# Kernel tuning notes

Measured on AMD Instinct MI355X. Metric: run time of the kernel, lower is better.

Reference implementation:

```python
import jax, jax.numpy as jnp
import numpy as np

B, S, H = 8, 1024, 16
DV = 1024      # video_input_dim
LAT = 1024     # latent_dim
DQ = LAT // H  # query_dim = 64
DH = 64        # head_dim


def setup_inputs() -> dict:
    key = jax.random.key(0)
    ks = jax.random.split(key, 12)
    sc = lambda fan_in: 1.0 / np.sqrt(fan_in)
    return {
        "input": jax.random.normal(ks[0], (B, S, DV), jnp.float32),
        "latent": jax.random.normal(ks[1], (B, S, LAT), jnp.float32),
        "attention_mask": jax.random.randint(ks[2], (B * H, S, S), 0, 2, jnp.int32),
        "Wq": jax.random.normal(ks[3], (LAT, H * DQ), jnp.float32) * sc(LAT),
        "bq": jnp.zeros((H * DQ,), jnp.float32),
        "Wk": jax.random.normal(ks[4], (DV, H * DQ), jnp.float32) * sc(DV),
        "bk": jnp.zeros((H * DQ,), jnp.float32),
        "Wv": jax.random.normal(ks[5], (DV, H * DH), jnp.float32) * sc(DV),
        "bv": jnp.zeros((H * DH,), jnp.float32),
        "Wo": jax.random.normal(ks[6], (H * DH, LAT), jnp.float32) * sc(H * DH),
        "bo": jnp.zeros((LAT,), jnp.float32),
    }


def reference(input, latent, attention_mask, Wq, bq, Wk, bk, Wv, bv, Wo, bo):
    b, s, _ = input.shape
    # projections -> [b, h, s, d]
    q = (latent @ Wq + bq).reshape(b, s, H, DQ).transpose(0, 2, 1, 3)
    k = (input @ Wk + bk).reshape(b, s, H, DQ).transpose(0, 2, 1, 3)
    v = (input @ Wv + bv).reshape(b, s, H, DH).transpose(0, 2, 1, 3)
    # [b, h, s, s] score matrix (materialized, as in the original bmm)
    scores = jnp.einsum("bhqd,bhkd->bhqk", q, k) / jnp.sqrt(jnp.float32(DQ))
    mask = attention_mask.reshape(b, H, s, s)
    scores = jnp.where(mask == 0, -jnp.inf, scores)
    weights = jax.nn.softmax(scores, axis=-1)
    out = jnp.einsum("bhqk,bhkd->bhqd", weights, v)  # [b, h, s, dh]
    out = out.transpose(0, 2, 1, 3).reshape(b, s, H * DH)
    return out @ Wo + bo
```

## Files before the change

### kernel.cpp

```cpp
#include <hip/hip_runtime.h>
#include <hip/hip_bf16.h>
#include <stdint.h>

typedef __bf16 bf16;
typedef __bf16 bf16x8 __attribute__((ext_vector_type(8)));
typedef float f32x4 __attribute__((ext_vector_type(4)));
typedef unsigned short u16;
typedef unsigned short u16x4 __attribute__((ext_vector_type(4)));


__global__ void convert_f32_bf16(const float* __restrict__ s0, bf16* __restrict__ d0,
                                 const float* __restrict__ s1, bf16* __restrict__ d1) {
    const float* src = blockIdx.y ? s1 : s0;
    bf16* dst = blockIdx.y ? d1 : d0;
    const int nchunk = (8 * 1024 * 1024) / 4;
    for (int c = blockIdx.x * blockDim.x + threadIdx.x; c < nchunk;
         c += gridDim.x * blockDim.x) {
        float4 v = *(const float4*)&src[(size_t)c * 4];
        u16x4 o;
        o[0] = __builtin_bit_cast(u16, (bf16)v.x);
        o[1] = __builtin_bit_cast(u16, (bf16)v.y);
        o[2] = __builtin_bit_cast(u16, (bf16)v.z);
        o[3] = __builtin_bit_cast(u16, (bf16)v.w);
        *(u16x4*)&dst[(size_t)c * 4] = o;
    }
}

__global__ void transpose4(const float* __restrict__ w0, const float* __restrict__ w1,
                           const float* __restrict__ w2, const float* __restrict__ w3,
                           bf16* __restrict__ t0, bf16* __restrict__ t1,
                           bf16* __restrict__ t2, bf16* __restrict__ t3) {
    __shared__ float tile[32][33];
    const float* src; bf16* dst;
    switch (blockIdx.z) {
        case 0:  src = w0; dst = t0; break;
        case 1:  src = w1; dst = t1; break;
        case 2:  src = w2; dst = t2; break;
        default: src = w3; dst = t3; break;
    }
    int tx = threadIdx.x, ty = threadIdx.y;
    int x = blockIdx.x * 32 + tx;
    int y = blockIdx.y * 32 + ty;
    #pragma unroll
    for (int j = 0; j < 32; j += 8)
        tile[ty + j][tx] = src[(size_t)(y + j) * 1024 + x];
    __syncthreads();
    int x2 = blockIdx.y * 32 + tx;
    int y2 = blockIdx.x * 32 + ty;
    #pragma unroll
    for (int j = 0; j < 32; j += 8)
        dst[(size_t)(y2 + j) * 1024 + x2] = (bf16)tile[tx][ty + j];
}

template<int MODE>
__global__ __launch_bounds__(256) void gemm_bt(const bf16* __restrict__ X,
                                               const bf16* __restrict__ Wt,
                                               const float* __restrict__ bias,
                                               void* __restrict__ outv) {
    __shared__ bf16 Al[128 * 40];
    __shared__ bf16 Bl[128 * 40];
    const int tid  = threadIdx.x;
    const int m0   = blockIdx.x * 128;
    const int n0   = blockIdx.y * 128;
    const int lane = tid & 63;
    const int wid  = tid >> 6;
    const int wm   = (wid & 1) * 64;
    const int wn   = (wid >> 1) * 64;
    const int l15  = lane & 15;
    const int quad = lane >> 4;

    f32x4 acc[4][4] = {};

    for (int kt = 0; kt < 1024; kt += 32) {
        __syncthreads();
        for (int c = tid; c < 512; c += 256) {
            int row = c >> 2, col = c & 3;
            *(bf16x8*)&Al[row * 40 + col * 8] =
                *(const bf16x8*)&X[(size_t)(m0 + row) * 1024 + kt + col * 8];
            *(bf16x8*)&Bl[row * 40 + col * 8] =
                *(const bf16x8*)&Wt[(size_t)(n0 + row) * 1024 + kt + col * 8];
        }
        __syncthreads();
        bf16x8 a[4], b[4];
        #pragma unroll
        for (int i = 0; i < 4; i++)
            a[i] = *(const bf16x8*)&Al[(wm + i * 16 + l15) * 40 + quad * 8];
        #pragma unroll
        for (int j = 0; j < 4; j++)
            b[j] = *(const bf16x8*)&Bl[(wn + j * 16 + l15) * 40 + quad * 8];
        #pragma unroll
        for (int i = 0; i < 4; i++)
            #pragma unroll
            for (int j = 0; j < 4; j++)
                acc[i][j] = __builtin_amdgcn_mfma_f32_16x16x32_bf16(a[i], b[j], acc[i][j], 0, 0, 0);
    }

    float bv[4];
    #pragma unroll
    for (int j = 0; j < 4; j++) bv[j] = bias[n0 + wn + j * 16 + l15];

    #pragma unroll
    for (int i = 0; i < 4; i++) {
        int mbase = m0 + wm + i * 16 + quad * 4;
        #pragma unroll
        for (int j = 0; j < 4; j++) {
            int n = n0 + wn + j * 16 + l15;
            if (MODE == 2) {
                bf16* out = (bf16*)outv;
                int b = mbase >> 10, s = mbase & 1023;
                int h = n >> 6, d = n & 63;
                u16x4 pack;
                #pragma unroll
                for (int r = 0; r < 4; r++) {
                    bf16 v = (bf16)(acc[i][j][r] + bv[j]);
                    pack[r] = __builtin_bit_cast(u16, v);
                }
                *(u16x4*)&out[(((size_t)(b * 16 + h)) * 64 + d) * 1024 + s] = pack;
            } else if (MODE == 1) {
                bf16* out = (bf16*)outv;
                #pragma unroll
                for (int r = 0; r < 4; r++) {
                    int m = mbase + r;
                    int b = m >> 10, s = m & 1023;
                    int h = n >> 6, d = n & 63;
                    out[(((size_t)(b * 16 + h)) * 1024 + s) * 64 + d] =
                        (bf16)(acc[i][j][r] + bv[j]);
                }
            } else {
                float* out = (float*)outv;
                #pragma unroll
                for (int r = 0; r < 4; r++) {
                    int m = mbase + r;
                    out[(size_t)m * 1024 + n] = acc[i][j][r] + bv[j];
                }
            }
        }
    }
}

__global__ __launch_bounds__(256) void attn(const bf16* __restrict__ Q,
                                            const bf16* __restrict__ K,
                                            const bf16* __restrict__ Vt,
                                            const int*  __restrict__ mask,
                                            bf16* __restrict__ O) {
    __shared__ bf16 Kl[32 * 72];
    __shared__ bf16 Vl[64 * 40];
    __shared__ bf16 Pl[4 * 16 * 40];

    const int tid  = threadIdx.x;
    const int bh   = blockIdx.y;
    const int q0   = blockIdx.x * 64;
    const int lane = tid & 63;
    const int w    = tid >> 6;
    const int l15  = lane & 15;
    const int quad = lane >> 4;
    const int qrow0 = q0 + w * 16;

    const bf16* Qb = Q + ((size_t)bh * 1024 + qrow0 + l15) * 64;
    bf16x8 qa0 = *(const bf16x8*)&Qb[quad * 8];
    bf16x8 qa1 = *(const bf16x8*)&Qb[32 + quad * 8];

    f32x4 o[4] = {};
    float mrow[4], lrow[4];
    #pragma unroll
    for (int r = 0; r < 4; r++) { mrow[r] = -1e30f; lrow[r] = 0.0f; }

    const int* mptr = mask + ((size_t)bh * 1024 + qrow0 + quad * 4) * 1024;

    for (int k0 = 0; k0 < 1024; k0 += 32) {
        __syncthreads();
        {
            int row = tid >> 3, ch = tid & 7;
            *(bf16x8*)&Kl[row * 72 + ch * 8] =
                *(const bf16x8*)&K[((size_t)bh * 1024 + k0 + row) * 64 + ch * 8];
            int d = tid >> 2, c2 = tid & 3;
            *(bf16x8*)&Vl[d * 40 + c2 * 8] =
                *(const bf16x8*)&Vt[((size_t)bh * 64 + d) * 1024 + k0 + c2 * 8];
        }
        __syncthreads();

        f32x4 s0 = {}, s1 = {};
        bf16x8 kb0a = *(const bf16x8*)&Kl[l15 * 72 + quad * 8];
        bf16x8 kb0b = *(const bf16x8*)&Kl[l15 * 72 + 32 + quad * 8];
        bf16x8 kb1a = *(const bf16x8*)&Kl[(16 + l15) * 72 + quad * 8];
        bf16x8 kb1b = *(const bf16x8*)&Kl[(16 + l15) * 72 + 32 + quad * 8];
        s0 = __builtin_amdgcn_mfma_f32_16x16x32_bf16(qa0, kb0a, s0, 0, 0, 0);
        s0 = __builtin_amdgcn_mfma_f32_16x16x32_bf16(qa1, kb0b, s0, 0, 0, 0);
        s1 = __builtin_amdgcn_mfma_f32_16x16x32_bf16(qa0, kb1a, s1, 0, 0, 0);
        s1 = __builtin_amdgcn_mfma_f32_16x16x32_bf16(qa1, kb1b, s1, 0, 0, 0);

        float sv0[4], sv1[4], pr0[4], pr1[4];
        #pragma unroll
        for (int r = 0; r < 4; r++) {
            int mk0 = mptr[(size_t)r * 1024 + k0 + l15];
            int mk1 = mptr[(size_t)r * 1024 + k0 + 16 + l15];
            sv0[r] = mk0 ? s0[r] * 0.125f : -1e30f;
            sv1[r] = mk1 ? s1[r] * 0.125f : -1e30f;
        }
        #pragma unroll
        for (int r = 0; r < 4; r++) {
            float tmax = fmaxf(sv0[r], sv1[r]);
            #pragma unroll
            for (int off = 1; off < 16; off <<= 1)
                tmax = fmaxf(tmax, __shfl_xor(tmax, off, 64));
            float mnew  = fmaxf(mrow[r], tmax);
            float alpha = __expf(mrow[r] - mnew);
            float p0 = __expf(sv0[r] - mnew);
            float p1 = __expf(sv1[r] - mnew);
            float ps = p0 + p1;
            #pragma unroll
            for (int off = 1; off < 16; off <<= 1)
                ps += __shfl_xor(ps, off, 64);
            lrow[r] = lrow[r] * alpha + ps;
            mrow[r] = mnew;
            pr0[r] = p0; pr1[r] = p1;
            #pragma unroll
            for (int nt = 0; nt < 4; nt++) o[nt][r] *= alpha;
        }

        bf16* Pw = &Pl[w * 16 * 40];
        #pragma unroll
        for (int r = 0; r < 4; r++) {
            Pw[(quad * 4 + r) * 40 + l15]      = (bf16)pr0[r];
            Pw[(quad * 4 + r) * 40 + 16 + l15] = (bf16)pr1[r];
        }
        __syncthreads();

        bf16x8 pa = *(const bf16x8*)&Pw[l15 * 40 + quad * 8];
        #pragma unroll
        for (int nt = 0; nt < 4; nt++) {
            bf16x8 vb = *(const bf16x8*)&Vl[(nt * 16 + l15) * 40 + quad * 8];
            o[nt] = __builtin_amdgcn_mfma_f32_16x16x32_bf16(pa, vb, o[nt], 0, 0, 0);
        }
    }

    const int b = bh >> 4, h = bh & 15;
    #pragma unroll
    for (int r = 0; r < 4; r++) {
        float inv = 1.0f / lrow[r];
        int s = qrow0 + quad * 4 + r;
        bf16* orow = O + ((size_t)(b * 1024 + s)) * 1024 + h * 64;
        #pragma unroll
        for (int nt = 0; nt < 4; nt++)
            orow[nt * 16 + l15] = (bf16)(o[nt][r] * inv);
    }
}

extern "C" void kernel_launch(void* const* d_in, const int* in_sizes, int n_in,
                              void* d_out, int out_size, void* d_ws, size_t ws_size,
                              hipStream_t stream) {
    const float* input  = (const float*)d_in[0];
    const float* latent = (const float*)d_in[1];
    const int*   mask   = (const int*)d_in[2];
    const float* Wq = (const float*)d_in[3];
    const float* bq = (const float*)d_in[4];
    const float* Wk = (const float*)d_in[5];
    const float* bk = (const float*)d_in[6];
    const float* Wv = (const float*)d_in[7];
    const float* bv = (const float*)d_in[8];
    const float* Wo = (const float*)d_in[9];
    const float* bo = (const float*)d_in[10];
    float* out = (float*)d_out;

    char* ws = (char*)d_ws;
    bf16* Xb  = (bf16*)(ws);
    bf16* Lb  = (bf16*)(ws + (16u << 20));
    bf16* Qh  = (bf16*)(ws + (32u << 20));
    bf16* Kh  = (bf16*)(ws + (48u << 20));
    bf16* Vt  = (bf16*)(ws + (64u << 20));
    bf16* Ob  = (bf16*)(ws + (80u << 20));
    bf16* Wqt = (bf16*)(ws + (96u << 20));
    bf16* Wkt = (bf16*)(ws + (98u << 20));
    bf16* Wvt = (bf16*)(ws + (100u << 20));
    bf16* Wot = (bf16*)(ws + (102u << 20));

    convert_f32_bf16<<<dim3(2048, 2, 1), 256, 0, stream>>>(input, Xb, latent, Lb);

    transpose4<<<dim3(32, 32, 4), dim3(32, 8, 1), 0, stream>>>(
        Wq, Wk, Wv, Wo, Wqt, Wkt, Wvt, Wot);

    dim3 g(64, 8, 1);
    gemm_bt<1><<<g, 256, 0, stream>>>(Lb, Wqt, bq, Qh);
    gemm_bt<1><<<g, 256, 0, stream>>>(Xb, Wkt, bk, Kh);
    gemm_bt<2><<<g, 256, 0, stream>>>(Xb, Wvt, bv, Vt);

    attn<<<dim3(16, 128, 1), 256, 0, stream>>>(Qh, Kh, Vt, mask, Ob);

    gemm_bt<0><<<g, 256, 0, stream>>>(Ob, Wot, bo, out);
}
```

Baseline: 980.8 us.

## Double-buffer attention K/V via direct-to-LDS loads and prefetch mask tiles

The attention kernel now processes 64-key tiles with double-buffered K/V shared-memory stages filled by global_load_lds, so the next tile's copy overlaps compute on the current one. Mask values for the next tile are prefetched into registers one iteration ahead. The per-tile barrier before the P·V step is dropped, since each wave only reads back its own P slice. The projection GEMM also switches to direct-to-LDS loads, which means removing the LDS row padding; this may add bank conflicts on fragment reads.

New measurement: 932.6 us. -4.9%, faster.

```diff
diff --git a/kernel.cpp b/kernel.cpp
--- a/kernel.cpp
+++ b/kernel.cpp
@@ -8,6 +8,12 @@
 typedef unsigned short u16;
 typedef unsigned short u16x4 __attribute__((ext_vector_type(4)));
 
+
+__device__ __forceinline__ void gld16(const bf16* g, bf16* l) {
+    __builtin_amdgcn_global_load_lds(
+        (const __attribute__((address_space(1))) void*)g,
+        (__attribute__((address_space(3))) void*)l, 16, 0, 0);
+}
 
 __global__ void convert_f32_bf16(const float* __restrict__ s0, bf16* __restrict__ d0,
                                  const float* __restrict__ s1, bf16* __restrict__ d1) {
@@ -57,15 +63,15 @@
                                                const bf16* __restrict__ Wt,
                                                const float* __restrict__ bias,
                                                void* __restrict__ outv) {
-    __shared__ bf16 Al[128 * 40];
-    __shared__ bf16 Bl[128 * 40];
+    __shared__ bf16 Al[128 * 32];
+    __shared__ bf16 Bl[128 * 32];
     const int tid  = threadIdx.x;
     const int m0   = blockIdx.x * 128;
     const int n0   = blockIdx.y * 128;
     const int lane = tid & 63;
-    const int wid  = tid >> 6;
-    const int wm   = (wid & 1) * 64;
-    const int wn   = (wid >> 1) * 64;
+    const int w    = tid >> 6;
+    const int wm   = (w & 1) * 64;
+    const int wn   = (w >> 1) * 64;
     const int l15  = lane & 15;
     const int quad = lane >> 4;
 
@@ -73,21 +79,21 @@
 
     for (int kt = 0; kt < 1024; kt += 32) {
         __syncthreads();
-        for (int c = tid; c < 512; c += 256) {
+        #pragma unroll
+        for (int t = 0; t < 2; t++) {
+            int c = (w * 2 + t) * 64 + lane;
             int row = c >> 2, col = c & 3;
-            *(bf16x8*)&Al[row * 40 + col * 8] =
-                *(const bf16x8*)&X[(size_t)(m0 + row) * 1024 + kt + col * 8];
-            *(bf16x8*)&Bl[row * 40 + col * 8] =
-                *(const bf16x8*)&Wt[(size_t)(n0 + row) * 1024 + kt + col * 8];
+            gld16(&X [(size_t)(m0 + row) * 1024 + kt + col * 8], &Al[(w * 2 + t) * 512]);
+            gld16(&Wt[(size_t)(n0 + row) * 1024 + kt + col * 8], &Bl[(w * 2 + t) * 512]);
         }
         __syncthreads();
         bf16x8 a[4], b[4];
         #pragma unroll
         for (int i = 0; i < 4; i++)
-            a[i] = *(const bf16x8*)&Al[(wm + i * 16 + l15) * 40 + quad * 8];
+            a[i] = *(const bf16x8*)&Al[(wm + i * 16 + l15) * 32 + quad * 8];
         #pragma unroll
         for (int j = 0; j < 4; j++)
-            b[j] = *(const bf16x8*)&Bl[(wn + j * 16 + l15) * 40 + quad * 8];
+            b[j] = *(const bf16x8*)&Bl[(wn + j * 16 + l15) * 32 + quad * 8];
         #pragma unroll
         for (int i = 0; i < 4; i++)
             #pragma unroll
@@ -129,10 +135,8 @@
             } else {
                 float* out = (float*)outv;
                 #pragma unroll
-                for (int r = 0; r < 4; r++) {
-                    int m = mbase + r;
-                    out[(size_t)m * 1024 + n] = acc[i][j][r] + bv[j];
-                }
+                for (int r = 0; r < 4; r++)
+                    out[(size_t)(mbase + r) * 1024 + n] = acc[i][j][r] + bv[j];
             }
         }
     }
@@ -143,9 +147,9 @@
                                             const bf16* __restrict__ Vt,
                                             const int*  __restrict__ mask,
                                             bf16* __restrict__ O) {
-    __shared__ bf16 Kl[32 * 72];
-    __shared__ bf16 Vl[64 * 40];
-    __shared__ bf16 Pl[4 * 16 * 40];
+    __shared__ bf16 Kl[2][4096];
+    __shared__ bf16 Vl[2][4096];
+    __shared__ bf16 Pl[4][16 * 68];
 
     const int tid  = threadIdx.x;
     const int bh   = blockIdx.y;
@@ -156,82 +160,114 @@
     const int quad = lane >> 4;
     const int qrow0 = q0 + w * 16;
 
-    const bf16* Qb = Q + ((size_t)bh * 1024 + qrow0 + l15) * 64;
+    const bf16* Qb  = Q  + ((size_t)bh * 1024 + qrow0 + l15) * 64;
+    const bf16* Kbh = K  + (size_t)bh * 1024 * 64;
+    const bf16* Vbh = Vt + (size_t)bh * 64 * 1024;
+    const int*  mptr = mask + ((size_t)bh * 1024 + qrow0 + quad * 4) * 1024;
+
     bf16x8 qa0 = *(const bf16x8*)&Qb[quad * 8];
     bf16x8 qa1 = *(const bf16x8*)&Qb[32 + quad * 8];
 
+    const int c0 = (w * 2 + 0) * 64 + lane;
+    const int c1 = (w * 2 + 1) * 64 + lane;
+
+    #define STAGE_KV(kk, buf)                                                        \
+        {                                                                            \
+            int h0 = c0 >> 8, r0 = (c0 >> 2) & 63, e0 = c0 & 3;                      \
+            int h1 = c1 >> 8, r1 = (c1 >> 2) & 63, e1 = c1 & 3;                      \
+            gld16(&Kbh[(size_t)((kk) + r0) * 64 + h0 * 32 + e0 * 8], &Kl[buf][(w * 2 + 0) * 512]); \
+            gld16(&Kbh[(size_t)((kk) + r1) * 64 + h1 * 32 + e1 * 8], &Kl[buf][(w * 2 + 1) * 512]); \
+            gld16(&Vbh[(size_t)r0 * 1024 + (kk) + h0 * 32 + e0 * 8], &Vl[buf][(w * 2 + 0) * 512]); \
+            gld16(&Vbh[(size_t)r1 * 1024 + (kk) + h1 * 32 + e1 * 8], &Vl[buf][(w * 2 + 1) * 512]); \
+        }
+
+    STAGE_KV(0, 0);
+    int mc[4][4];
+    #pragma unroll
+    for (int r = 0; r < 4; r++)
+        #pragma unroll
+        for (int t = 0; t < 4; t++)
+            mc[r][t] = mptr[(size_t)r * 1024 + t * 16 + l15];
+
     f32x4 o[4] = {};
     float mrow[4], lrow[4];
     #pragma unroll
     for (int r = 0; r < 4; r++) { mrow[r] = -1e30f; lrow[r] = 0.0f; }
 
-    const int* mptr = mask + ((size_t)bh * 1024 + qrow0 + quad * 4) * 1024;
-
-    for (int k0 = 0; k0 < 1024; k0 += 32) {
+    bf16* Pw = &Pl[w][0];
+
+    for (int it = 0; it < 16; it++) {
         __syncthreads();
-        {
-            int row = tid >> 3, ch = tid & 7;
-            *(bf16x8*)&Kl[row * 72 + ch * 8] =
-                *(const bf16x8*)&K[((size_t)bh * 1024 + k0 + row) * 64 + ch * 8];
-            int d = tid >> 2, c2 = tid & 3;
-            *(bf16x8*)&Vl[d * 40 + c2 * 8] =
-                *(const bf16x8*)&Vt[((size_t)bh * 64 + d) * 1024 + k0 + c2 * 8];
-        }
-        __syncthreads();
-
-        f32x4 s0 = {}, s1 = {};
-        bf16x8 kb0a = *(const bf16x8*)&Kl[l15 * 72 + quad * 8];
-        bf16x8 kb0b = *(const bf16x8*)&Kl[l15 * 72 + 32 + quad * 8];
-        bf16x8 kb1a = *(const bf16x8*)&Kl[(16 + l15) * 72 + quad * 8];
-        bf16x8 kb1b = *(const bf16x8*)&Kl[(16 + l15) * 72 + 32 + quad * 8];
-        s0 = __builtin_amdgcn_mfma_f32_16x16x32_bf16(qa0, kb0a, s0, 0, 0, 0);
-        s0 = __builtin_amdgcn_mfma_f32_16x16x32_bf16(qa1, kb0b, s0, 0, 0, 0);
-        s1 = __builtin_amdgcn_mfma_f32_16x16x32_bf16(qa0, kb1a, s1, 0, 0, 0);
-        s1 = __builtin_amdgcn_mfma_f32_16x16x32_bf16(qa1, kb1b, s1, 0, 0, 0);
-
-        float sv0[4], sv1[4], pr0[4], pr1[4];
+        const int cur = it & 1, nxt = cur ^ 1;
+        const int kn = ((it + 1) & 15) * 64;
+
+        STAGE_KV(kn, nxt);
+        int mn[4][4];
+        #pragma unroll
+        for (int r = 0; r < 4; r++)
+            #pragma unroll
+            for (int t = 0; t < 4; t++)
+                mn[r][t] = mptr[(size_t)r * 1024 + kn + t * 16 + l15];
+
+        f32x4 s[4];
+        #pragma unroll
+        for (int t = 0; t < 4; t++) {
+            bf16x8 kb0 = *(const bf16x8*)&Kl[cur][(t * 16 + l15) * 32 + quad * 8];
+            bf16x8 kb1 = *(const bf16x8*)&Kl[cur][(64 + t * 16 + l15) * 32 + quad * 8];
+            f32x4 z = {};
+            z = __builtin_amdgcn_mfma_f32_16x16x32_bf16(qa0, kb0, z, 0, 0, 0);
+            z = __builtin_amdgcn_mfma_f32_16x16x32_bf16(qa1, kb1, z, 0, 0, 0);
+            s[t] = z;
+        }
+
+        float sv[4][4], p[4][4];
+        #pragma unroll
+        for (int t = 0; t < 4; t++)
+            #pragma unroll
+            for (int r = 0; r < 4; r++)
+                sv[t][r] = mc[r][t] ? s[t][r] * 0.125f : -1e30f;
+
         #pragma unroll
         for (int r = 0; r < 4; r++) {
-            int mk0 = mptr[(size_t)r * 1024 + k0 + l15];
-            int mk1 = mptr[(size_t)r * 1024 + k0 + 16 + l15];
-            sv0[r] = mk0 ? s0[r] * 0.125f : -1e30f;
-            sv1[r] = mk1 ? s1[r] * 0.125f : -1e30f;
-        }
-        #pragma unroll
-        for (int r = 0; r < 4; r++) {
-            float tmax = fmaxf(sv0[r], sv1[r]);
+            float tmax = fmaxf(fmaxf(sv[0][r], sv[1][r]), fmaxf(sv[2][r], sv[3][r]));
             #pragma unroll
             for (int off = 1; off < 16; off <<= 1)
                 tmax = fmaxf(tmax, __shfl_xor(tmax, off, 64));
             float mnew  = fmaxf(mrow[r], tmax);
             float alpha = __expf(mrow[r] - mnew);
-            float p0 = __expf(sv0[r] - mnew);
-            float p1 = __expf(sv1[r] - mnew);
-            float ps = p0 + p1;
+            float ps = 0.0f;
+            #pragma unroll
+            for (int t = 0; t < 4; t++) { p[t][r] = __expf(sv[t][r] - mnew); ps += p[t][r]; }
             #pragma unroll
             for (int off = 1; off < 16; off <<= 1)
                 ps += __shfl_xor(ps, off, 64);
             lrow[r] = lrow[r] * alpha + ps;
             mrow[r] = mnew;
-            pr0[r] = p0; pr1[r] = p1;
             #pragma unroll
             for (int nt = 0; nt < 4; nt++) o[nt][r] *= alpha;
         }
 
-        bf16* Pw = &Pl[w * 16 * 40];
-        #pragma unroll
-        for (int r = 0; r < 4; r++) {
-            Pw[(quad * 4 + r) * 40 + l15]      = (bf16)pr0[r];
-            Pw[(quad * 4 + r) * 40 + 16 + l15] = (bf16)pr1[r];
-        }
-        __syncthreads();
-
-        bf16x8 pa = *(const bf16x8*)&Pw[l15 * 40 + quad * 8];
+        #pragma unroll
+        for (int r = 0; r < 4; r++)
+            #pragma unroll
+            for (int t = 0; t < 4; t++)
+                Pw[(quad * 4 + r) * 68 + t * 16 + l15] = (bf16)p[t][r];
+
+        bf16x8 pa0 = *(const bf16x8*)&Pw[l15 * 68 + quad * 8];
+        bf16x8 pa1 = *(const bf16x8*)&Pw[l15 * 68 + 32 + quad * 8];
         #pragma unroll
         for (int nt = 0; nt < 4; nt++) {
-            bf16x8 vb = *(const bf16x8*)&Vl[(nt * 16 + l15) * 40 + quad * 8];
-            o[nt] = __builtin_amdgcn_mfma_f32_16x16x32_bf16(pa, vb, o[nt], 0, 0, 0);
-        }
+            bf16x8 vb0 = *(const bf16x8*)&Vl[cur][(nt * 16 + l15) * 32 + quad * 8];
+            bf16x8 vb1 = *(const bf16x8*)&Vl[cur][(64 + nt * 16 + l15) * 32 + quad * 8];
+            o[nt] = __builtin_amdgcn_mfma_f32_16x16x32_bf16(pa0, vb0, o[nt], 0, 0, 0);
+            o[nt] = __builtin_amdgcn_mfma_f32_16x16x32_bf16(pa1, vb1, o[nt], 0, 0, 0);
+        }
+
+        #pragma unroll
+        for (int r = 0; r < 4; r++)
+            #pragma unroll
+            for (int t = 0; t < 4; t++)
+                mc[r][t] = mn[r][t];
     }
 
     const int b = bh >> 4, h = bh & 15;
@@ -244,6 +280,7 @@
         for (int nt = 0; nt < 4; nt++)
             orow[nt * 16 + l15] = (bf16)(o[nt][r] * inv);
     }
+    #undef STAGE_KV
 }
 
 extern "C" void kernel_launch(void* const* d_in, const int* in_sizes, int n_in,
```
